# Kernel tuning notes

Hardware: AMD Instinct MI355X
Metric: run time of the kernel (lower is better)

The kernel has to match this reference:

```python
import jax, jax.numpy as jnp
import numpy as np

N = 20000      # nodes
E = 160000     # edges
F_IN = 64      # node_feature_dim
HID = 256      # hidden_dim (= per-head out_channels, concat=False)
HEADS = 4
OUT = 2
BN_EPS = 1e-5


def setup_inputs() -> dict:
    key = jax.random.key(0)
    ks = jax.random.split(key, 24)
    s = 0.02

    def w(k, shape):
        return jax.random.normal(k, shape, jnp.float32) * s

    return {
        "node_feature": jax.random.normal(ks[0], (N, F_IN), jnp.float32),
        "edge_index": jax.random.randint(ks[1], (2, E), 0, N, jnp.int32),
        # layer 1 (in=F_IN)
        "wq1": w(ks[2], (F_IN, HEADS * HID)), "bq1": w(ks[3], (HEADS * HID,)),
        "wk1": w(ks[4], (F_IN, HEADS * HID)), "bk1": w(ks[5], (HEADS * HID,)),
        "wv1": w(ks[6], (F_IN, HEADS * HID)), "bv1": w(ks[7], (HEADS * HID,)),
        "ws1": w(ks[8], (F_IN, HID)),        "bs1": w(ks[9], (HID,)),
        # layer 2 (in=HID)
        "wq2": w(ks[10], (HID, HEADS * HID)), "bq2": w(ks[11], (HEADS * HID,)),
        "wk2": w(ks[12], (HID, HEADS * HID)), "bk2": w(ks[13], (HEADS * HID,)),
        "wv2": w(ks[14], (HID, HEADS * HID)), "bv2": w(ks[15], (HEADS * HID,)),
        "ws2": w(ks[16], (HID, HID)),         "bs2": w(ks[17], (HID,)),
        # batch norm affine
        "bn_gamma": jnp.ones((HID,), jnp.float32) + w(ks[18], (HID,)),
        "bn_beta": w(ks[19], (HID,)),
        # final linear
        "lin_w": w(ks[20], (HID, OUT)), "lin_b": w(ks[21], (OUT,)),
    }


def _transformer_conv(x, src, dst, wq, bq, wk, bk, wv, bv, ws, bs):
    """PyG TransformerConv, heads=HEADS, concat=False (mean over heads), root_weight."""
    n = x.shape[0]
    q = (x @ wq + bq).reshape(n, HEADS, HID)   # [N,H,C]
    k = (x @ wk + bk).reshape(n, HEADS, HID)
    v = (x @ wv + bv).reshape(n, HEADS, HID)
    # per-edge attention logits: q_i . k_j / sqrt(C)   (message j->i, i = dst)
    alpha = jnp.einsum('ehc,ehc->eh', q[dst], k[src]) / jnp.sqrt(jnp.float32(HID))  # [E,H]
    # scatter-softmax over incoming edges of each target node
    m = jax.ops.segment_max(alpha, dst, num_segments=n)
    m = jnp.where(jnp.isfinite(m), m, 0.0)  # nodes with no in-edges
    ex = jnp.exp(alpha - m[dst])
    denom = jax.ops.segment_sum(ex, dst, num_segments=n)
    a = ex / (denom[dst] + 1e-16)                          # [E,H]
    out = jax.ops.segment_sum(v[src] * a[..., None], dst, num_segments=n)  # [N,H,C]
    return out.mean(axis=1) + x @ ws + bs                  # concat=False -> head mean; + skip


def reference(node_feature, edge_index,
              wq1, bq1, wk1, bk1, wv1, bv1, ws1, bs1,
              wq2, bq2, wk2, bk2, wv2, bv2, ws2, bs2,
              bn_gamma, bn_beta, lin_w, lin_b):
    src, dst = edge_index[0], edge_index[1]
    x = _transformer_conv(node_feature, src, dst, wq1, bq1, wk1, bk1, wv1, bv1, ws1, bs1)
    x = _transformer_conv(x, src, dst, wq2, bq2, wk2, bk2, wv2, bv2, ws2, bs2)
    # BatchNorm1d (training mode: batch statistics, biased variance)
    mu = x.mean(axis=0)
    var = jnp.mean(jnp.square(x - mu), axis=0)
    x = bn_gamma * (x - mu) / jnp.sqrt(var + BN_EPS) + bn_beta
    rsu_embedding = x[0:1]                     # [1, HID]
    logits = jax.nn.relu(x @ lin_w + lin_b)    # [N, OUT]
    action_prob = jax.nn.softmax(logits, axis=1)
    return (action_prob, rsu_embedding)
```

## Files before the change

### kernel.cpp

```cpp
#include <hip/hip_runtime.h>
#include <hip/hip_bf16.h>
#include <math.h>

#define DI __device__ __forceinline__

constexpr int NN   = 20000;
constexpr int NE   = 160000;
constexpr int FIN  = 64;
constexpr int HIDC = 256;

typedef __attribute__((ext_vector_type(8))) short short8;
typedef __attribute__((ext_vector_type(4))) float f32x4;

DI float bf2f(unsigned short u) { return __uint_as_float(((unsigned)u) << 16); }

DI void gld16(const void* g, void* l) {
  __builtin_amdgcn_global_load_lds((const __attribute__((address_space(1))) unsigned*)g,
                                   (__attribute__((address_space(3))) unsigned*)l, 16, 0, 0);
}

__global__ void k_prep(const float* __restrict__ x, __hip_bfloat16* __restrict__ xb,
                       const int* __restrict__ dst, int* __restrict__ deg) {
  int gid = blockIdx.x * 256 + threadIdx.x;
  if (gid < NN * FIN) xb[gid] = __float2bfloat16(x[gid]);
  if (gid < NE) atomicAdd(&deg[dst[gid]], 1);
}

__global__ void k_scan(const int* __restrict__ deg, int* __restrict__ offs,
                       int* __restrict__ cursor, int n_) {
  __shared__ int part[1024];
  int tid = threadIdx.x;
  const int CH = (n_ + 1023) >> 10;
  int base = tid * CH;
  int s = 0;
  for (int i = 0; i < CH; ++i) { int idx = base + i; if (idx < n_) s += deg[idx]; }
  part[tid] = s;
  __syncthreads();
  for (int off = 1; off < 1024; off <<= 1) {
    int v = (tid >= off) ? part[tid - off] : 0;
    __syncthreads();
    part[tid] += v;
    __syncthreads();
  }
  int run = (tid == 0) ? 0 : part[tid - 1];
  for (int i = 0; i < CH; ++i) {
    int idx = base + i;
    if (idx < n_) { offs[idx] = run; cursor[idx] = run; run += deg[idx]; }
  }
  if (tid == 1023) offs[n_] = run;
}

__global__ void k_scatter(const int* __restrict__ dst, int* __restrict__ cursor,
                          int* __restrict__ eid, int e_) {
  int e = blockIdx.x * blockDim.x + threadIdx.x;
  if (e < e_) {
    int p = atomicAdd(&cursor[dst[e]], 1);
    eid[p] = e;
  }
}

__global__ void k_sortsse(const int* __restrict__ offs, int* __restrict__ eid,
                          const int* __restrict__ src, int* __restrict__ sse, int n_) {
  int n = blockIdx.x * 256 + threadIdx.x;
  if (n >= n_) return;
  int s0 = offs[n], s1 = offs[n + 1];
  for (int i = s0 + 1; i < s1; ++i) {
    int v = eid[i];
    int j = i - 1;
    while (j >= s0 && eid[j] > v) { eid[j + 1] = eid[j]; --j; }
    eid[j + 1] = v;
  }
  for (int i = s0; i < s1; ++i) sse[i] = src[eid[i]];
}

__global__ void k_tr(const float* __restrict__ wq, const float* __restrict__ wk,
                     float* __restrict__ WqT, float* __restrict__ WkT, int IN_) {
  int gid = blockIdx.x * 256 + threadIdx.x;
  if (gid >= 1024 * IN_) return;
  int k = gid % IN_, j = gid / IN_;
  WqT[gid] = wq[(size_t)k * 1024 + j];
  WkT[gid] = wk[(size_t)k * 1024 + j];
}

template <int IN>
__global__ void k_mfill(const float* __restrict__ WqT, const float* __restrict__ WkT,
                        const float* __restrict__ bq, const float* __restrict__ bk,
                        const float* __restrict__ ws, const float* __restrict__ bs,
                        __hip_bfloat16* __restrict__ Wt, float* __restrict__ biasp) {
  constexpr int YW = 4 * IN;
  constexpr int CPB = 256 / IN;
  int k = threadIdx.x % IN;
  int sub = threadIdx.x / IN;
  int c = blockIdx.x * CPB + sub;
  float val = 0.f, bval = 0.f;
  if (c < YW) {
    int h = c / IN, i = c % IN;
    const float* wqp = WqT + (size_t)(h * 256) * IN + k;
    const float* wkp = WkT + (size_t)(h * 256) * IN + i;
    float s = 0.f;
#pragma unroll 4
    for (int j = 0; j < 256; ++j) s = fmaf(wqp[(size_t)j * IN], wkp[(size_t)j * IN], s);
    val = s;
  } else if (c < YW + 256) {
    int sc = c - YW;
    val = ws[(size_t)k * 256 + sc];
    bval = bs[sc];
  } else if (c < YW + 260) {
    int h = c - (YW + 256);
    const float* wqp = WqT + (size_t)(h * 256) * IN + k;
    const float* bkp = bk + h * 256;
    float s = 0.f;
#pragma unroll 4
    for (int j = 0; j < 256; ++j) s = fmaf(wqp[(size_t)j * IN], bkp[j], s);
    val = s;
    if (k == 0) {
      float bb = 0.f;
      for (int j = 0; j < 256; ++j) bb = fmaf(bq[h * 256 + j], bk[h * 256 + j], bb);
      bval = bb;
    }
  } else if (c < YW + 264) {
    int h = c - (YW + 260);
    const float* wkp = WkT + (size_t)(h * 256) * IN + k;
    const float* bqp = bq + h * 256;
    float s = 0.f;
#pragma unroll 4
    for (int j = 0; j < 256; ++j) s = fmaf(wkp[(size_t)j * IN], bqp[j], s);
    val = s;
  }
  Wt[(size_t)c * IN + k] = __float2bfloat16(val);
  if (k == 0) biasp[c] = bval;
}

template <int IN>
__global__ void k_pack2(const float* __restrict__ wv, const float* __restrict__ bv,
                        __hip_bfloat16* __restrict__ Wt2, float* __restrict__ bias2) {
  constexpr int K2 = 4 * IN;
  int gid = blockIdx.x * 256 + threadIdx.x;
  int col = gid / K2, k = gid % K2;
  int h = k / IN, d = k % IN;
  Wt2[gid] = __float2bfloat16(0.25f * wv[(size_t)d * 1024 + h * 256 + col]);
  if (k == 0)
    bias2[col] = 0.25f * (bv[col] + bv[256 + col] + bv[512 + col] + bv[768 + col]);
}

template <int IN>
__global__ __launch_bounds__(64, 2) void k_gemm1(
    const __hip_bfloat16* __restrict__ X, const __hip_bfloat16* __restrict__ Wt,
    const float* __restrict__ biasp,
    __hip_bfloat16* __restrict__ Ybuf, float* __restrict__ skipf,
    float* __restrict__ CDbuf, int nrows, int NCB, int NCH, int TPC, int RT) {
  __shared__ char lds[16384 + 2304];
  const int l = threadIdx.x;
  constexpr int K = IN;
  constexpr int YW = 4 * IN;
  const int nwg = NCB * NCH;
  const int per = nwg >> 3;
  const int w = (blockIdx.x & 7) * per + (blockIdx.x >> 3);
  const int chunk = w / NCB;
  const int ct = w % NCB;
  const int bn = ct * 64;
  const int t0 = chunk * TPC;
  int t1 = t0 + TPC; if (t1 > RT) t1 = RT;
  constexpr int KT = K / 64;
  constexpr int NS = K / 32;

  const int lm = l & 15, lk = l >> 4;

  short8 bfr[4 * NS];
  {
    const __hip_bfloat16* bp = Wt + (size_t)(bn + lm) * K + lk * 8;
#pragma unroll
    for (int n = 0; n < 4; ++n)
#pragma unroll
      for (int s = 0; s < NS; ++s)
        bfr[n * NS + s] = *(const short8*)(bp + (size_t)n * 16 * K + s * 32);
  }
  float bia[4];
#pragma unroll
  for (int n = 0; n < 4; ++n) bia[n] = biasp[bn + n * 16 + lm];

  const int mode = (bn < YW) ? 0 : ((bn < YW + 256) ? 1 : 2);

  const int jrow = l >> 3;
  const int cslot = (l & 7) ^ jrow;
  auto STAGE = [&](int buf, int t, int kt) {
    char* db = lds + buf * 8192;
#pragma unroll
    for (int j = 0; j < 8; ++j) {
      int r = t * 64 + j * 8 + jrow;
      if (r >= nrows) r = nrows - 1;
      gld16(X + (size_t)r * K + kt * 64 + cslot * 8, db + j * 1024 + l * 16);
    }
  };

  int buf = 0;
  STAGE(0, t0, 0);
  for (int t = t0; t < t1; ++t) {
    f32x4 acc[4][4] = {};
#pragma unroll
    for (int kt = 0; kt < KT; ++kt) {
      int nt = t, nk = kt + 1;
      if (nk == KT) { nt = (t + 1 < t1) ? t + 1 : t; nk = 0; }
      STAGE(buf ^ 1, nt, nk);
      asm volatile("s_waitcnt vmcnt(8)" ::: "memory");
      const char* db = lds + buf * 8192;
#pragma unroll
      for (int s2 = 0; s2 < 2; ++s2) {
        short8 a[4];
#pragma unroll
        for (int m = 0; m < 4; ++m) {
          int row = m * 16 + lm;
          a[m] = *(const short8*)(db + row * 128 + (((s2 * 4 + lk) ^ (lm & 7)) * 16));
        }
#pragma unroll
        for (int m = 0; m < 4; ++m)
#pragma unroll
          for (int n = 0; n < 4; ++n)
            acc[m][n] = __builtin_amdgcn_mfma_f32_16x16x32_bf16(
                a[m], bfr[n * NS + kt * 2 + s2], acc[m][n], 0, 0, 0);
      }
      buf ^= 1;
    }

    const int tbase = t * 64;
    if (mode == 0) {
      char* sc = lds + 16384;
      const int srow = l >> 2, qc = l & 3;
#pragma unroll
      for (int m = 0; m < 4; ++m) {
#pragma unroll
        for (int n = 0; n < 4; ++n)
#pragma unroll
          for (int r = 0; r < 4; ++r)
            *(__hip_bfloat16*)(sc + (lk * 4 + r) * 144 + (n * 16 + lm) * 2) =
                __float2bfloat16(acc[m][n][r] + bia[n]);
        const char* sr = sc + srow * 144 + qc * 32;
        short8 ta = *(const short8*)(sr);
        short8 tb = *(const short8*)(sr + 16);
        int grow = tbase + m * 16 + srow;
        if (grow < nrows) {
          ushort* o = (ushort*)Ybuf + (size_t)grow * YW + bn + qc * 16;
          *(short8*)o = ta;
          *(short8*)(o + 8) = tb;
        }
      }
    } else if (mode == 1) {
      const int cb = bn - YW;
#pragma unroll
      for (int m = 0; m < 4; ++m)
#pragma unroll
        for (int n = 0; n < 4; ++n)
#pragma unroll
          for (int r = 0; r < 4; ++r) {
            int row = tbase + m * 16 + lk * 4 + r;
            if (row < nrows) skipf[(size_t)row * HIDC + cb + n * 16 + lm] = acc[m][n][r] + bia[n];
          }
    } else {
#pragma unroll
      for (int m = 0; m < 4; ++m)
#pragma unroll
        for (int n = 0; n < 4; ++n) {
          int cl = n * 16 + lm;
          if (cl < 8) {
#pragma unroll
            for (int r = 0; r < 4; ++r) {
              int row = tbase + m * 16 + lk * 4 + r;
              if (row < nrows) CDbuf[(size_t)row * 8 + cl] = acc[m][n][r] + bia[n];
            }
          }
        }
    }
  }
  asm volatile("s_waitcnt vmcnt(0)" ::: "memory");
}

template <int IN>
__global__ __launch_bounds__(256) void k_attn(
    const __hip_bfloat16* __restrict__ Ybuf, const __hip_bfloat16* __restrict__ Xs,
    const float* __restrict__ CD, const int* __restrict__ offs,
    const int* __restrict__ sse, __hip_bfloat16* __restrict__ Zbuf,
    float* __restrict__ Abuf) {
  constexpr int DPL = IN / 16;
  constexpr int YW = 4 * IN;
  int n = blockIdx.x * 4 + (threadIdx.x >> 6);
  if (n >= NN) return;
  int lane = threadIdx.x & 63;
  int h = lane >> 4, j = lane & 15;
  int s0 = offs[n];
  int deg = offs[n + 1] - s0;
  ushort* zr = (ushort*)Zbuf + (size_t)n * YW + h * IN + j * DPL;
  if (deg == 0) {
#pragma unroll
    for (int d = 0; d < DPL; ++d) zr[d] = 0;
    if (lane == 0) Abuf[n] = 0.f;
    return;
  }

  float y[DPL];
  {
    const ushort* yr = (const ushort*)Ybuf + (size_t)n * YW + h * IN + j * DPL;
    if constexpr (IN == 256) {
      short8 y0 = *(const short8*)yr;
      short8 y1 = *(const short8*)(yr + 8);
#pragma unroll
      for (int d = 0; d < 8; ++d) {
        y[d] = bf2f((unsigned short)y0[d]);
        y[8 + d] = bf2f((unsigned short)y1[d]);
      }
    } else {
      short4 yv = *(const short4*)yr;
      y[0] = bf2f((unsigned short)yv.x);
      y[1] = bf2f((unsigned short)yv.y);
      y[2] = bf2f((unsigned short)yv.z);
      y[3] = bf2f((unsigned short)yv.w);
    }
  }
  float C = CD[(size_t)n * 8 + h];
  float acc[DPL] = {};
  float denom = 0.f;
  const int* se = sse + s0;
  const ushort* xb = (const ushort*)Xs;

#define LOADE(P, E)                                                     \
  {                                                                     \
    int e_ = (E);                                                       \
    int s_ = se[(e_ < deg) ? e_ : 0];                                   \
    const ushort* xp_ = xb + (size_t)s_ * IN + j * DPL;                 \
    if constexpr (IN == 256) {                                          \
      P##0 = *(const short8*)xp_;                                       \
      P##1 = *(const short8*)(xp_ + 8);                                 \
    } else {                                                            \
      P##s = *(const short4*)xp_;                                       \
    }                                                                   \
    P##D = CD[(size_t)s_ * 8 + 4 + h];                                  \
  }

#define COMPE(P, E)                                                     \
  {                                                                     \
    float xf[DPL];                                                      \
    if constexpr (IN == 256) {                                          \
      _Pragma("unroll") for (int d = 0; d < 8; ++d) {                   \
        xf[d] = bf2f((unsigned short)P##0[d]);                          \
        xf[8 + d] = bf2f((unsigned short)P##1[d]);                      \
      }                                                                 \
    } else {                                                            \
      xf[0] = bf2f((unsigned short)P##s.x);                             \
      xf[1] = bf2f((unsigned short)P##s.y);                             \
      xf[2] = bf2f((unsigned short)P##s.z);                             \
      xf[3] = bf2f((unsigned short)P##s.w);                             \
    }                                                                   \
    float p_ = 0.f;                                                     \
    _Pragma("unroll") for (int d = 0; d < DPL; ++d) p_ = fmaf(y[d], xf[d], p_); \
    p_ += __shfl_xor(p_, 1);                                            \
    p_ += __shfl_xor(p_, 2);                                            \
    p_ += __shfl_xor(p_, 4);                                            \
    p_ += __shfl_xor(p_, 8);                                            \
    float w_ = ((E) < deg) ? __expf((p_ + C + P##D) * 0.0625f) : 0.f;   \
    denom += w_;                                                        \
    _Pragma("unroll") for (int d = 0; d < DPL; ++d) acc[d] = fmaf(w_, xf[d], acc[d]); \
  }

  short8 A0, A1, B0, B1;
  short4 As, Bs;
  float AD, BD;
  (void)As; (void)Bs; (void)A0; (void)A1; (void)B0; (void)B1;
  LOADE(A, 0);
  for (int e = 0; e < deg; e += 2) {
    LOADE(B, e + 1);
    COMPE(A, e);
    LOADE(A, e + 2);
    COMPE(B, e + 1);
  }
#undef LOADE
#undef COMPE

  float dinv = 1.f / (denom + 1e-16f);
  if constexpr (IN == 256) {
    short8 o0, o1;
#pragma unroll
    for (int d = 0; d < 8; ++d) {
      o0[d] = (short)__bfloat16_as_ushort(__float2bfloat16(acc[d] * dinv));
      o1[d] = (short)__bfloat16_as_ushort(__float2bfloat16(acc[8 + d] * dinv));
    }
    *(short8*)zr = o0;
    *(short8*)(zr + 8) = o1;
  } else {
    short4 o;
    o.x = (short)__bfloat16_as_ushort(__float2bfloat16(acc[0] * dinv));
    o.y = (short)__bfloat16_as_ushort(__float2bfloat16(acc[1] * dinv));
    o.z = (short)__bfloat16_as_ushort(__float2bfloat16(acc[2] * dinv));
    o.w = (short)__bfloat16_as_ushort(__float2bfloat16(acc[3] * dinv));
    *(short4*)zr = o;
  }
  if (lane == 0) Abuf[n] = 1.f;
}

template <int K2, bool F32OUT>
__global__ __launch_bounds__(64, 2) void k_gemm2(
    const __hip_bfloat16* __restrict__ Z, const __hip_bfloat16* __restrict__ Wt2,
    const float* __restrict__ bias2, const float* __restrict__ Abuf,
    const float* __restrict__ skipf, void* __restrict__ outp, int nrows) {
  __shared__ char lds[16384];
  const int l = threadIdx.x;
  const int tile = blockIdx.x >> 1;
  const int bn = (blockIdx.x & 1) * 128;
  constexpr int KT = K2 / 64;
  const int lm = l & 15, lk = l >> 4;
  const int jrow = l >> 3, cslot = (l & 7) ^ jrow;

  float bia[8];
#pragma unroll
  for (int n = 0; n < 8; ++n) bia[n] = bias2[bn + n * 16 + lm];

  auto STAGE = [&](int buf, int ch) {
    char* db = lds + buf * 8192;
#pragma unroll
    for (int jj = 0; jj < 8; ++jj) {
      int r = tile * 64 + jj * 8 + jrow;
      if (r >= nrows) r = nrows - 1;
      gld16(Z + (size_t)r * K2 + ch * 64 + cslot * 8, db + jj * 1024 + l * 16);
    }
  };

  f32x4 acc[4][8] = {};
  int buf = 0;
  STAGE(0, 0);
  for (int ch = 0; ch < KT; ++ch) {
    short8 bfr[8][2];
    const __hip_bfloat16* bp = Wt2 + (size_t)(bn + lm) * K2 + ch * 64 + lk * 8;
#pragma unroll
    for (int n = 0; n < 8; ++n)
#pragma unroll
      for (int s2 = 0; s2 < 2; ++s2)
        bfr[n][s2] = *(const short8*)(bp + (size_t)n * 16 * K2 + s2 * 32);
    STAGE(buf ^ 1, (ch + 1 < KT) ? ch + 1 : ch);
    asm volatile("s_waitcnt vmcnt(8)" ::: "memory");
    const char* db = lds + buf * 8192;
#pragma unroll
    for (int s2 = 0; s2 < 2; ++s2) {
      short8 a[4];
#pragma unroll
      for (int m = 0; m < 4; ++m) {
        int row = m * 16 + lm;
        a[m] = *(const short8*)(db + row * 128 + (((s2 * 4 + lk) ^ (lm & 7)) * 16));
      }
#pragma unroll
      for (int m = 0; m < 4; ++m)
#pragma unroll
        for (int n = 0; n < 8; ++n)
          acc[m][n] = __builtin_amdgcn_mfma_f32_16x16x32_bf16(a[m], bfr[n][s2], acc[m][n], 0, 0, 0);
    }
    buf ^= 1;
  }

  const int tbase = tile * 64;
#pragma unroll
  for (int m = 0; m < 4; ++m)
#pragma unroll
    for (int r = 0; r < 4; ++r) {
      int row = tbase + m * 16 + lk * 4 + r;
      if (row >= nrows) continue;
      float af = Abuf[row];
#pragma unroll
      for (int n = 0; n < 8; ++n) {
        int col = bn + n * 16 + lm;
        float v = acc[m][n][r] + af * bia[n] + skipf[(size_t)row * HIDC + col];
        if constexpr (F32OUT)
          ((float*)outp)[(size_t)row * HIDC + col] = v;
        else
          ((ushort*)outp)[(size_t)row * HIDC + col] = __bfloat16_as_ushort(__float2bfloat16(v));
      }
    }
  asm volatile("s_waitcnt vmcnt(0)" ::: "memory");
}

__global__ void k_bnstats(const float* __restrict__ x, float* __restrict__ psum,
                          float* __restrict__ psumsq) {
  int t = threadIdx.x, b = blockIdx.x;
  float s = 0.f, s2 = 0.f;
  for (int r = b; r < NN; r += 256) {
    float vv = x[(size_t)r * HIDC + t];
    s += vv; s2 += vv * vv;
  }
  psum[b * HIDC + t] = s;
  psumsq[b * HIDC + t] = s2;
}

__global__ void k_bnred(const float* __restrict__ psum, const float* __restrict__ psumsq,
                        float* __restrict__ sums, float* __restrict__ sumsq) {
  int t = threadIdx.x;
  float s = 0.f, s2 = 0.f;
  for (int b = 0; b < 256; ++b) { s += psum[b * HIDC + t]; s2 += psumsq[b * HIDC + t]; }
  sums[t] = s;
  sumsq[t] = s2;
}

__global__ __launch_bounds__(256) void k_final(
    const float* __restrict__ x, const float* __restrict__ sums, const float* __restrict__ sumsq,
    const float* __restrict__ gamma, const float* __restrict__ beta,
    const float* __restrict__ lw, const float* __restrict__ lb,
    float* __restrict__ out, int n_) {
  int sub = threadIdx.x >> 6, lane = threadIdx.x & 63;
  int n = blockIdx.x * 4 + sub;
  if (n >= n_) return;
  int c = lane * 4;
  float4 sm  = *(const float4*)(sums + c);
  float4 sq  = *(const float4*)(sumsq + c);
  const float inv_n = 1.f / (float)n_;
  float mu0 = sm.x * inv_n, mu1 = sm.y * inv_n, mu2 = sm.z * inv_n, mu3 = sm.w * inv_n;
  float r0 = 1.f / sqrtf(fmaxf(sq.x * inv_n - mu0 * mu0, 0.f) + 1e-5f);
  float r1 = 1.f / sqrtf(fmaxf(sq.y * inv_n - mu1 * mu1, 0.f) + 1e-5f);
  float r2 = 1.f / sqrtf(fmaxf(sq.z * inv_n - mu2 * mu2, 0.f) + 1e-5f);
  float r3 = 1.f / sqrtf(fmaxf(sq.w * inv_n - mu3 * mu3, 0.f) + 1e-5f);
  const float* xr = x + (size_t)n * HIDC;
  float4 xv = *(const float4*)(xr + c);
  float4 gv = *(const float4*)(gamma + c);
  float4 bv = *(const float4*)(beta + c);
  float y0 = gv.x * (xv.x - mu0) * r0 + bv.x;
  float y1 = gv.y * (xv.y - mu1) * r1 + bv.y;
  float y2 = gv.z * (xv.z - mu2) * r2 + bv.z;
  float y3 = gv.w * (xv.w - mu3) * r3 + bv.w;
  float4 wa = *(const float4*)(lw + (size_t)c * 2);
  float4 wb = *(const float4*)(lw + (size_t)c * 2 + 4);
  float p0 = y0 * wa.x + y1 * wa.z + y2 * wb.x + y3 * wb.z;
  float p1 = y0 * wa.y + y1 * wa.w + y2 * wb.y + y3 * wb.w;
#pragma unroll
  for (int off = 32; off > 0; off >>= 1) {
    p0 += __shfl_xor(p0, off);
    p1 += __shfl_xor(p1, off);
  }
  if (n == 0) *(float4*)(out + (size_t)NN * 2 + c) = make_float4(y0, y1, y2, y3);
  if (lane == 0) {
    float l0 = fmaxf(p0 + lb[0], 0.f);
    float l1 = fmaxf(p1 + lb[1], 0.f);
    float m = fmaxf(l0, l1);
    float e0 = expf(l0 - m), e1 = expf(l1 - m);
    float inv = 1.f / (e0 + e1);
    out[(size_t)n * 2 + 0] = e0 * inv;
    out[(size_t)n * 2 + 1] = e1 * inv;
  }
}

extern "C" void kernel_launch(void* const* d_in, const int* in_sizes, int n_in,
                              void* d_out, int out_size, void* d_ws, size_t ws_size,
                              hipStream_t stream) {
  const float* x0  = (const float*)d_in[0];
  const int*   ei  = (const int*)d_in[1];
  const float* wq1 = (const float*)d_in[2];  const float* bq1 = (const float*)d_in[3];
  const float* wk1 = (const float*)d_in[4];  const float* bk1 = (const float*)d_in[5];
  const float* wv1 = (const float*)d_in[6];  const float* bv1 = (const float*)d_in[7];
  const float* ws1 = (const float*)d_in[8];  const float* bs1 = (const float*)d_in[9];
  const float* wq2 = (const float*)d_in[10]; const float* bq2 = (const float*)d_in[11];
  const float* wk2 = (const float*)d_in[12]; const float* bk2 = (const float*)d_in[13];
  const float* wv2 = (const float*)d_in[14]; const float* bv2 = (const float*)d_in[15];
  const float* ws2 = (const float*)d_in[16]; const float* bs2 = (const float*)d_in[17];
  const float* gam = (const float*)d_in[18]; const float* bet = (const float*)d_in[19];
  const float* lw  = (const float*)d_in[20]; const float* lb  = (const float*)d_in[21];
  const int* srcv = ei;
  const int* dstv = ei + NE;

  char* p = (char*)d_ws;
  auto take = [&](size_t bytes) {
    char* r = p;
    p += (bytes + 255) & ~(size_t)255;
    return r;
  };
  __hip_bfloat16* Ybuf = (__hip_bfloat16*)take((size_t)NN * 1024 * 2);
  __hip_bfloat16* Zbuf = (__hip_bfloat16*)take((size_t)NN * 1024 * 2);
  float* skipf = (float*)take((size_t)NN * HIDC * 4);
  float* x3    = (float*)take((size_t)NN * HIDC * 4);
  __hip_bfloat16* x0b = (__hip_bfloat16*)take((size_t)NN * FIN * 2);
  __hip_bfloat16* x2b = (__hip_bfloat16*)take((size_t)NN * HIDC * 2);
  float* CDbuf = (float*)take((size_t)NN * 8 * 4);
  float* Abuf  = (float*)take((size_t)NN * 4);
  __hip_bfloat16* Wt1a = (__hip_bfloat16*)take((size_t)576 * 64 * 2);
  __hip_bfloat16* Wt1b = (__hip_bfloat16*)take((size_t)1344 * 256 * 2);
  float* bias1a = (float*)take(576 * 4);
  float* bias1b = (float*)take(1344 * 4);
  __hip_bfloat16* Wt2a = (__hip_bfloat16*)take((size_t)256 * 256 * 2);
  __hip_bfloat16* Wt2b = (__hip_bfloat16*)take((size_t)256 * 1024 * 2);
  float* bias2a = (float*)take(256 * 4);
  float* bias2b = (float*)take(256 * 4);
  float* WqTa = (float*)take((size_t)1024 * 64 * 4);
  float* WkTa = (float*)take((size_t)1024 * 64 * 4);
  float* WqTb = (float*)take((size_t)1024 * 256 * 4);
  float* WkTb = (float*)take((size_t)1024 * 256 * 4);
  float* psum  = (float*)take(256 * HIDC * 4);
  float* psumsq= (float*)take(256 * HIDC * 4);
  float* bnbuf = (float*)take(2 * HIDC * 4);
  int* deg    = (int*)take((size_t)NN * 4);
  int* offs   = (int*)take((size_t)(NN + 1) * 4);
  int* cursor = (int*)take((size_t)NN * 4);
  int* eidb   = (int*)take((size_t)NE * 4);
  int* sse    = (int*)take((size_t)NE * 4);
  if ((size_t)(p - (char*)d_ws) > ws_size) return;

  float* sums  = bnbuf;
  float* sumsq = bnbuf + HIDC;

  hipMemsetAsync(deg, 0, (size_t)NN * 4, stream);
  k_prep<<<(NN * FIN + 255) / 256, 256, 0, stream>>>(x0, x0b, dstv, deg);
  k_scan<<<1, 1024, 0, stream>>>(deg, offs, cursor, NN);
  k_scatter<<<(NE + 255) / 256, 256, 0, stream>>>(dstv, cursor, eidb, NE);
  k_sortsse<<<(NN + 255) / 256, 256, 0, stream>>>(offs, eidb, srcv, sse, NN);

  k_tr<<<(1024 * 64 + 255) / 256, 256, 0, stream>>>(wq1, wk1, WqTa, WkTa, 64);
  k_mfill<64><<<144, 256, 0, stream>>>(WqTa, WkTa, bq1, bk1, ws1, bs1, Wt1a, bias1a);
  k_pack2<64><<<256, 256, 0, stream>>>(wv1, bv1, Wt2a, bias2a);
  k_tr<<<(1024 * 256 + 255) / 256, 256, 0, stream>>>(wq2, wk2, WqTb, WkTb, 256);
  k_mfill<256><<<1344, 256, 0, stream>>>(WqTb, WkTb, bq2, bk2, ws2, bs2, Wt1b, bias1b);
  k_pack2<256><<<1024, 256, 0, stream>>>(wv2, bv2, Wt2b, bias2b);

  const int RT  = (NN + 63) / 64;
  const int NCH = 40;
  const int TPC = (RT + NCH - 1) / NCH;
  const int AG = (NN + 3) / 4;
  const int G2 = RT * 2;

  k_gemm1<64><<<9 * NCH, 64, 0, stream>>>(x0b, Wt1a, bias1a, Ybuf, skipf, CDbuf, NN, 9, NCH, TPC, RT);
  k_attn<64><<<AG, 256, 0, stream>>>(Ybuf, x0b, CDbuf, offs, sse, Zbuf, Abuf);
  k_gemm2<256, false><<<G2, 64, 0, stream>>>(Zbuf, Wt2a, bias2a, Abuf, skipf, x2b, NN);
  k_gemm1<256><<<21 * NCH, 64, 0, stream>>>(x2b, Wt1b, bias1b, Ybuf, skipf, CDbuf, NN, 21, NCH, TPC, RT);
  k_attn<256><<<AG, 256, 0, stream>>>(Ybuf, x2b, CDbuf, offs, sse, Zbuf, Abuf);
  k_gemm2<1024, true><<<G2, 64, 0, stream>>>(Zbuf, Wt2b, bias2b, Abuf, skipf, x3, NN);
  k_bnstats<<<256, 256, 0, stream>>>(x3, psum, psumsq);
  k_bnred<<<1, 256, 0, stream>>>(psum, psumsq, sums, sumsq);
  k_final<<<(NN + 3) / 4, 256, 0, stream>>>(x3, sums, sumsq, gam, bet, lw, lb, (float*)d_out, NN);
}
```

Baseline: 374.3 us.

## Shrink gemm2 tiles to 32x64, double-buffer B fragments, remap blocks across XCDs

k_gemm2 now uses 32-row by 64-column output tiles instead of 64x128, which quadruples the grid and halves LDS use so more blocks fit per CU. B-weight register fragments are double-buffered and prefetched one K-chunk ahead alongside the A stage, unrolled by two. Block IDs are remapped so consecutive logical tiles land on the same XCD for L2 locality. Smaller tiles mean less reuse per load, so Z and the weights get re-read more often, and the loop assumes KT is even.

```diff
diff --git a/kernel.cpp b/kernel.cpp
--- a/kernel.cpp
+++ b/kernel.cpp
@@ -396,73 +396,93 @@
 }
 
 template <int K2, bool F32OUT>
-__global__ __launch_bounds__(64, 2) void k_gemm2(
+__global__ __launch_bounds__(64, 3) void k_gemm2(
     const __hip_bfloat16* __restrict__ Z, const __hip_bfloat16* __restrict__ Wt2,
     const float* __restrict__ bias2, const float* __restrict__ Abuf,
     const float* __restrict__ skipf, void* __restrict__ outp, int nrows) {
-  __shared__ char lds[16384];
+  __shared__ char lds[8192];
   const int l = threadIdx.x;
-  const int tile = blockIdx.x >> 1;
-  const int bn = (blockIdx.x & 1) * 128;
+  int bid = blockIdx.x;
+  {
+    int nwg = gridDim.x;
+    int q8 = nwg >> 3, r8 = nwg & 7;
+    int xcd = bid & 7, idx = bid >> 3;
+    bid = (xcd < r8 ? xcd * (q8 + 1) : r8 * (q8 + 1) + (xcd - r8) * q8) + idx;
+  }
+  const int tile = bid >> 2;
+  const int bn = (bid & 3) * 64;
   constexpr int KT = K2 / 64;
   const int lm = l & 15, lk = l >> 4;
   const int jrow = l >> 3, cslot = (l & 7) ^ jrow;
 
-  float bia[8];
-#pragma unroll
-  for (int n = 0; n < 8; ++n) bia[n] = bias2[bn + n * 16 + lm];
-
-  auto STAGE = [&](int buf, int ch) {
-    char* db = lds + buf * 8192;
-#pragma unroll
-    for (int jj = 0; jj < 8; ++jj) {
-      int r = tile * 64 + jj * 8 + jrow;
+  float bia[4];
+#pragma unroll
+  for (int n = 0; n < 4; ++n) bia[n] = bias2[bn + n * 16 + lm];
+
+  const __hip_bfloat16* bp = Wt2 + (size_t)(bn + lm) * K2 + lk * 8;
+
+  auto ISSUE_A = [&](int buf, int ch) {
+    char* db = lds + buf * 4096;
+#pragma unroll
+    for (int jj = 0; jj < 4; ++jj) {
+      int r = tile * 32 + jj * 8 + jrow;
       if (r >= nrows) r = nrows - 1;
       gld16(Z + (size_t)r * K2 + ch * 64 + cslot * 8, db + jj * 1024 + l * 16);
     }
   };
 
-  f32x4 acc[4][8] = {};
-  int buf = 0;
-  STAGE(0, 0);
-  for (int ch = 0; ch < KT; ++ch) {
-    short8 bfr[8][2];
-    const __hip_bfloat16* bp = Wt2 + (size_t)(bn + lm) * K2 + ch * 64 + lk * 8;
-#pragma unroll
-    for (int n = 0; n < 8; ++n)
-#pragma unroll
-      for (int s2 = 0; s2 < 2; ++s2)
-        bfr[n][s2] = *(const short8*)(bp + (size_t)n * 16 * K2 + s2 * 32);
-    STAGE(buf ^ 1, (ch + 1 < KT) ? ch + 1 : ch);
-    asm volatile("s_waitcnt vmcnt(8)" ::: "memory");
-    const char* db = lds + buf * 8192;
-#pragma unroll
-    for (int s2 = 0; s2 < 2; ++s2) {
-      short8 a[4];
-#pragma unroll
-      for (int m = 0; m < 4; ++m) {
-        int row = m * 16 + lm;
-        a[m] = *(const short8*)(db + row * 128 + (((s2 * 4 + lk) ^ (lm & 7)) * 16));
-      }
-#pragma unroll
-      for (int m = 0; m < 4; ++m)
-#pragma unroll
-        for (int n = 0; n < 8; ++n)
-          acc[m][n] = __builtin_amdgcn_mfma_f32_16x16x32_bf16(a[m], bfr[n][s2], acc[m][n], 0, 0, 0);
-    }
-    buf ^= 1;
-  }
-
-  const int tbase = tile * 64;
-#pragma unroll
-  for (int m = 0; m < 4; ++m)
+  short8 bA[4][2], bB[4][2];
+#define ISSUE_B(DST, CH)                                                    \
+  {                                                                         \
+    int ch_ = (CH);                                                         \
+    _Pragma("unroll") for (int n = 0; n < 4; ++n)                           \
+      _Pragma("unroll") for (int s2 = 0; s2 < 2; ++s2)                      \
+        DST[n][s2] = *(const short8*)(bp + (size_t)n * 16 * K2 + ch_ * 64 + s2 * 32); \
+  }
+
+  f32x4 acc[2][4] = {};
+#define COMPUTE(BSRC, BUF)                                                  \
+  {                                                                         \
+    const char* db = lds + (BUF) * 4096;                                    \
+    _Pragma("unroll") for (int s2 = 0; s2 < 2; ++s2) {                      \
+      short8 a[2];                                                          \
+      _Pragma("unroll") for (int m = 0; m < 2; ++m) {                       \
+        int row = m * 16 + lm;                                              \
+        a[m] = *(const short8*)(db + row * 128 + (((s2 * 4 + lk) ^ (lm & 7)) * 16)); \
+      }                                                                     \
+      _Pragma("unroll") for (int m = 0; m < 2; ++m)                         \
+        _Pragma("unroll") for (int n = 0; n < 4; ++n)                       \
+          acc[m][n] = __builtin_amdgcn_mfma_f32_16x16x32_bf16(a[m], BSRC[n][s2], acc[m][n], 0, 0, 0); \
+    }                                                                       \
+  }
+
+  ISSUE_B(bA, 0);
+  ISSUE_A(0, 0);
+  for (int ch = 0; ch < KT; ch += 2) {
+    int c1 = ch + 1;
+    ISSUE_B(bB, c1);
+    ISSUE_A(1, c1);
+    asm volatile("s_waitcnt vmcnt(12)" ::: "memory");
+    COMPUTE(bA, 0);
+    int c2 = (ch + 2 < KT) ? ch + 2 : c1;
+    ISSUE_B(bA, c2);
+    ISSUE_A(0, c2);
+    asm volatile("s_waitcnt vmcnt(12)" ::: "memory");
+    COMPUTE(bB, 1);
+  }
+#undef ISSUE_B
+#undef COMPUTE
+
+  const int tbase = tile * 32;
+#pragma unroll
+  for (int m = 0; m < 2; ++m)
 #pragma unroll
     for (int r = 0; r < 4; ++r) {
       int row = tbase + m * 16 + lk * 4 + r;
       if (row >= nrows) continue;
       float af = Abuf[row];
 #pragma unroll
-      for (int n = 0; n < 8; ++n) {
+      for (int n = 0; n < 4; ++n) {
         int col = bn + n * 16 + lm;
         float v = acc[m][n][r] + af * bia[n] + skipf[(size_t)row * HIDC + col];
         if constexpr (F32OUT)
@@ -615,7 +635,8 @@
   const int NCH = 40;
   const int TPC = (RT + NCH - 1) / NCH;
   const int AG = (NN + 3) / 4;
-  const int G2 = RT * 2;
+  const int NRT32 = (NN + 31) / 32;
+  const int G2 = NRT32 * 4;
 
   k_gemm1<64><<<9 * NCH, 64, 0, stream>>>(x0b, Wt1a, bias1a, Ybuf, skipf, CDbuf, NN, 9, NCH, TPC, RT);
   k_attn<64><<<AG, 256, 0, stream>>>(Ybuf, x0b, CDbuf, offs, sse, Zbuf, Abuf);
```

Result: slower. 382.3 us (+2.1%).
